# Kernel tuning notes

Measured on AMD Instinct MI355X. Metric: run time of the kernel, lower is better.

## Reference

```python
import jax, jax.numpy as jnp
import numpy as np

N_QUBITS = 8
EMBED_DIM = 1024
FFN_DIM = 4096


def setup_inputs() -> dict:
    key = jax.random.key(0)
    ks = jax.random.split(key, 6)
    x = jax.random.normal(ks[0], (8, 4096, EMBED_DIM), dtype=jnp.float32)
    # trainable RY rotation angles, one per wire (torchquantum RY has_params=True)
    theta = jax.random.normal(ks[1], (N_QUBITS,), dtype=jnp.float32)
    # torch nn.Linear params: W [out, in], b [out]
    W1 = jax.random.normal(ks[2], (FFN_DIM, N_QUBITS), dtype=jnp.float32) / np.sqrt(N_QUBITS)
    b1 = jnp.zeros((FFN_DIM,), dtype=jnp.float32)
    W2 = jax.random.normal(ks[3], (EMBED_DIM, FFN_DIM), dtype=jnp.float32) / np.sqrt(FFN_DIM)
    b2 = jnp.zeros((EMBED_DIM,), dtype=jnp.float32)
    return {"x": x, "theta": theta, "W1": W1, "b1": b1, "W2": W2, "b2": b2}


def reference(x, theta, W1, b1, W2, b2):
    # Quantum layer: per token, encoder resets state to |0..0>, applies RX(x_i)
    # on wire i, then trainable RY(theta_i), then measures <Z_i>. The circuit has
    # no entangling gates, so it factorizes per wire with the closed form:
    #   <Z_i> = cos(theta_i) * cos(x[..., i])
    # (RY(t)RX(a)|0> gives <Z> = cos t * cos a). Vectorized over batch and seq.
    q = jnp.cos(theta) * jnp.cos(x[..., :N_QUBITS])   # [B, S, n_qubits]
    # dropout is identity in eval mode
    h = jax.nn.relu(jnp.einsum('bsq,fq->bsf', q, W1) + b1)  # [B, S, ffn]
    out = jnp.einsum('bsf,ef->bse', h, W2) + b2              # [B, S, embed]
    return out
```

## Files before the change

### kernel.cpp

```cpp
#include <hip/hip_runtime.h>
#include <cstdint>
#include <cstddef>


#define M_TOT 32768L
#define N_DIM 1024
#define K_DIM 4096
#define BM 256
#define BN 256
#define BK 64
#define NT_K (K_DIM / BK)
#define CM_MAX 16384L

typedef __attribute__((ext_vector_type(8))) short short8;
typedef __attribute__((ext_vector_type(4))) float f32x4;

__device__ __forceinline__ uint16_t f2bf(float f) {
  uint32_t u = __builtin_bit_cast(uint32_t, f);
  uint32_t r = (u + 0x7fffu + ((u >> 16) & 1u)) >> 16;
  return (uint16_t)r;
}

__device__ __forceinline__ void gload_lds16(const void* gsrc, void* ldst) {
  __builtin_amdgcn_global_load_lds(
      (const __attribute__((address_space(1))) void*)gsrc,
      (__attribute__((address_space(3))) void*)ldst, 16, 0, 0);
}

__global__ __launch_bounds__(256) void prep_w2(const float* __restrict__ W2,
                                               uint16_t* __restrict__ W2sw) {
  long idx = (long)blockIdx.x * 256 + threadIdx.x;
  long e8 = idx * 8;
  int e = (int)(e8 >> 12);
  int k = (int)(e8 & 4095);
  float4 v0 = *(const float4*)(W2 + e8);
  float4 v1 = *(const float4*)(W2 + e8 + 4);
  union { uint16_t u[8]; uint4 v; } pk;
  pk.u[0] = f2bf(v0.x); pk.u[1] = f2bf(v0.y); pk.u[2] = f2bf(v0.z); pk.u[3] = f2bf(v0.w);
  pk.u[4] = f2bf(v1.x); pk.u[5] = f2bf(v1.y); pk.u[6] = f2bf(v1.z); pk.u[7] = f2bf(v1.w);
  int sg = ((k >> 3) & 7) ^ (e & 7);
  uint16_t* dst = W2sw + (long)e * 4096 + (k & ~63) + sg * 8;
  *(uint4*)dst = pk.v;
}

__global__ __launch_bounds__(256) void h_kernel(const float* __restrict__ x,
                                                const float* __restrict__ theta,
                                                const float* __restrict__ W1,
                                                const float* __restrict__ b1,
                                                uint16_t* __restrict__ Hsw) {
  __shared__ float qs[32][8];
  int tid = threadIdx.x;
  long m0 = (long)blockIdx.x * 32;
  int g = blockIdx.y * 256 + tid;
  int f0 = g * 8;

  {
    int t = tid >> 3, i = tid & 7;
    qs[t][i] = __cosf(theta[i]) * cosf(x[(m0 + t) * 1024 + i]);
  }
  __syncthreads();

  float4 w[16];
#pragma unroll
  for (int j = 0; j < 8; ++j) {
    w[2 * j]     = *(const float4*)(W1 + (long)(f0 + j) * 8);
    w[2 * j + 1] = *(const float4*)(W1 + (long)(f0 + j) * 8 + 4);
  }
  float bb[8];
#pragma unroll
  for (int j = 0; j < 8; ++j) bb[j] = b1[f0 + j];

  int blk = (g >> 3) * 64;
  int gw = g & 7;

#pragma unroll 4
  for (int t = 0; t < 32; ++t) {
    long m = m0 + t;
    float q0 = qs[t][0], q1 = qs[t][1], q2 = qs[t][2], q3 = qs[t][3];
    float q4 = qs[t][4], q5 = qs[t][5], q6 = qs[t][6], q7 = qs[t][7];
    union { uint16_t u[8]; uint4 v; } pk;
#pragma unroll
    for (int j = 0; j < 8; ++j) {
      float h = bb[j];
      h += q0 * w[2 * j].x + q1 * w[2 * j].y + q2 * w[2 * j].z + q3 * w[2 * j].w;
      h += q4 * w[2 * j + 1].x + q5 * w[2 * j + 1].y + q6 * w[2 * j + 1].z + q7 * w[2 * j + 1].w;
      h = fmaxf(h, 0.0f);
      pk.u[j] = f2bf(h);
    }
    int sg = gw ^ ((int)m & 7);
    *(uint4*)&Hsw[m * K_DIM + blk + sg * 8] = pk.v;
  }
}

__global__ __launch_bounds__(512, 2) void gemm_kernel(const uint16_t* __restrict__ Hsw,
                                                      const uint16_t* __restrict__ W2sw,
                                                      const float* __restrict__ b2,
                                                      float* __restrict__ out) {
  __shared__ uint16_t LA[2 * BM * BK];
  __shared__ uint16_t LB[2 * BN * BK];

  int nwg = gridDim.x;
  int bid = blockIdx.x;
  int sw = bid;
  if ((nwg & 7) == 0) { int cpx = nwg >> 3; sw = (bid & 7) * cpx + (bid >> 3); }
  const int NTN = N_DIM / BN;
  int mt = sw / NTN;
  int nt = sw - mt * NTN;
  long m0 = (long)mt * BM;
  int n0 = nt * BN;

  int tid = threadIdx.x;
  int lane = tid & 63;
  int wave_m = (tid >> 6) >> 2;
  int wave_n = (tid >> 6) & 3;
  int wmB = wave_m * 128;
  int wnB = wave_n * 64;

  int r  = lane & 15;
  int kq = lane >> 4;
  int xr = r & 7;

  int rowS = tid >> 3;
  int colS = (tid & 7) * 8;
  const uint16_t* srcA = Hsw  + (m0 + rowS) * K_DIM + colS;
  const uint16_t* srcB = W2sw + ((long)(n0 + rowS)) * K_DIM + colS;
  int ldsWB = (tid & ~63) * 8;

#define STAGE_A(p, h, j, t) \
  gload_lds16(srcA + (long)((h)*128 + (j)*64) * K_DIM + (t)*BK, \
              &LA[(p)*16384 + ((h)*128 + (j)*64)*BK + ldsWB])
#define STAGE_B(p, h, j, t) \
  gload_lds16(srcB + (long)((h)*128 + (j)*64) * K_DIM + (t)*BK, \
              &LB[(p)*16384 + ((h)*128 + (j)*64)*BK + ldsWB])

#define BAR() do { asm volatile("" ::: "memory"); __builtin_amdgcn_s_barrier(); \
                   asm volatile("" ::: "memory"); } while (0)
#define SGB(m_, n_) __builtin_amdgcn_sched_group_barrier((m_), (n_), 0)

#define LDA_F(p, mf_, ks_) \
  (*(const short8*)&LA[(p)*16384 + (wmB + (mf_)*16 + r)*BK + ((((ks_)*4 + kq) ^ xr)*8)])
#define LDB_F(p, nf_, ks_) \
  (*(const short8*)&LB[(p)*16384 + (wnB + (nf_)*16 + r)*BK + ((((ks_)*4 + kq) ^ xr)*8)])

#define MFMA_Q(AARR, BARR, mh, nh) do { \
    _Pragma("unroll") for (int i_ = 0; i_ < 4; ++i_) \
    _Pragma("unroll") for (int j_ = 0; j_ < 2; ++j_) \
    _Pragma("unroll") for (int ks_ = 0; ks_ < 2; ++ks_) \
      acc[(mh)*4 + i_][(nh)*2 + j_] = __builtin_amdgcn_mfma_f32_16x16x32_bf16( \
          AARR[i_][ks_], BARR[j_][ks_], acc[(mh)*4 + i_][(nh)*2 + j_], 0, 0, 0); \
  } while (0)

#define READ_B1V(p) do { \
    _Pragma("unroll") for (int j_ = 0; j_ < 2; ++j_) \
    _Pragma("unroll") for (int ks_ = 0; ks_ < 2; ++ks_) \
      b1v[j_][ks_] = LDB_F(p, 2 + j_, ks_); \
  } while (0)
#define READ_A1(p) do { \
    _Pragma("unroll") for (int i_ = 0; i_ < 4; ++i_) \
    _Pragma("unroll") for (int ks_ = 0; ks_ < 2; ++ks_) \
      a1[i_][ks_] = LDA_F(p, 4 + i_, ks_); \
  } while (0)
#define READ_A0(pn) do { \
    _Pragma("unroll") for (int i_ = 0; i_ < 4; ++i_) \
    _Pragma("unroll") for (int ks_ = 0; ks_ < 2; ++ks_) \
      a0[i_][ks_] = LDA_F(pn, i_, ks_); \
  } while (0)
#define READ_B0(pn) do { \
    _Pragma("unroll") for (int j_ = 0; j_ < 2; ++j_) \
    _Pragma("unroll") for (int ks_ = 0; ks_ < 2; ++ks_) \
      b0[j_][ks_] = LDB_F(pn, j_, ks_); \
  } while (0)

  f32x4 acc[8][4];
#pragma unroll
  for (int i = 0; i < 8; ++i)
#pragma unroll
    for (int j = 0; j < 4; ++j) acc[i][j] = (f32x4){0.f, 0.f, 0.f, 0.f};

  short8 a0[4][2];
  short8 a1[4][2];
  short8 b0[2][2];
  short8 b1v[2][2];

#pragma unroll
  for (int h = 0; h < 2; ++h)
#pragma unroll
    for (int j = 0; j < 2; ++j) STAGE_A(0, h, j, 0);
#pragma unroll
  for (int h = 0; h < 2; ++h)
#pragma unroll
    for (int j = 0; j < 2; ++j) STAGE_B(0, h, j, 0);
#pragma unroll
  for (int h = 0; h < 2; ++h)
#pragma unroll
    for (int j = 0; j < 2; ++j) STAGE_A(1, h, j, 1);
#pragma unroll
  for (int h = 0; h < 2; ++h)
#pragma unroll
    for (int j = 0; j < 2; ++j) STAGE_B(1, h, j, 1);
  asm volatile("s_waitcnt vmcnt(8)" ::: "memory");
  BAR();
  READ_A0(0);
  READ_B0(0);

#pragma unroll 2
  for (int u = 0; u < NT_K; ++u) {
    int p = u & 1;
    int tc = (u + 2 < NT_K) ? (u + 2) : (NT_K - 1);

    MFMA_Q(a0, b0, 0, 0);
    READ_B1V(p);
    READ_A1(p);
#pragma unroll
    for (int s_ = 0; s_ < 12; ++s_) { SGB(0x8, 1); SGB(0x100, 1); }
    SGB(0x8, 4);
    BAR();

    STAGE_A(p, 0, 0, tc); STAGE_A(p, 1, 0, tc);
    STAGE_B(p, 0, 0, tc); STAGE_B(p, 0, 1, tc);
    STAGE_B(p, 1, 0, tc); STAGE_B(p, 1, 1, tc);
    MFMA_Q(a0, b1v, 0, 1);
    MFMA_Q(a1, b1v, 1, 1);
#pragma unroll
    for (int s_ = 0; s_ < 6; ++s_) { SGB(0x10, 1); SGB(0x8, 5); }
    SGB(0x8, 2);
    if (u < NT_K - 2)       { asm volatile("s_waitcnt vmcnt(6)" ::: "memory"); }
    else if (u == NT_K - 2) { asm volatile("s_waitcnt vmcnt(0)" ::: "memory"); }
    BAR();

    READ_A0(p ^ 1);
    MFMA_Q(a1, b0, 1, 0);
    READ_B0(p ^ 1);
    STAGE_A(p, 0, 1, tc); STAGE_A(p, 1, 1, tc);
#pragma unroll
    for (int s_ = 0; s_ < 8; ++s_) { SGB(0x8, 1); SGB(0x100, 1); }
    SGB(0x10, 2); SGB(0x8, 8); SGB(0x100, 4);
    BAR();
  }

  float bb[4];
#pragma unroll
  for (int nf = 0; nf < 4; ++nf) bb[nf] = b2[n0 + wnB + nf * 16 + r];
  long mbase = m0 + wmB + kq * 4;
#pragma unroll
  for (int mf = 0; mf < 8; ++mf) {
#pragma unroll
    for (int nf = 0; nf < 4; ++nf) {
      int n = n0 + wnB + nf * 16 + r;
#pragma unroll
      for (int rg = 0; rg < 4; ++rg) {
        out[(mbase + mf * 16 + rg) * N_DIM + n] = acc[mf][nf][rg] + bb[nf];
      }
    }
  }
#undef STAGE_A
#undef STAGE_B
#undef BAR
#undef SGB
#undef LDA_F
#undef LDB_F
#undef MFMA_Q
#undef READ_B1V
#undef READ_A1
#undef READ_A0
#undef READ_B0
}

extern "C" void kernel_launch(void* const* d_in, const int* in_sizes, int n_in,
                              void* d_out, int out_size, void* d_ws, size_t ws_size,
                              hipStream_t stream) {
  const float* x     = (const float*)d_in[0];
  const float* theta = (const float*)d_in[1];
  const float* W1    = (const float*)d_in[2];
  const float* b1    = (const float*)d_in[3];
  const float* W2    = (const float*)d_in[4];
  const float* b2    = (const float*)d_in[5];
  float* out = (float*)d_out;

  const size_t W2SW_BYTES = (size_t)N_DIM * K_DIM * 2;
  uint16_t* W2sw = (uint16_t*)d_ws;
  uint16_t* Hsw  = (uint16_t*)((char*)d_ws + W2SW_BYTES);

  size_t avail = ws_size > W2SW_BYTES ? ws_size - W2SW_BYTES : 0;
  long CM = (long)(avail / ((size_t)K_DIM * 2));
  CM &= ~255L;
  if (CM > CM_MAX) CM = CM_MAX;
  if (CM < 256) CM = 256;

  prep_w2<<<2048, 256, 0, stream>>>(W2, W2sw);

  for (long m0 = 0; m0 < M_TOT; m0 += CM) {
    long mc = M_TOT - m0;
    if (mc > CM) mc = CM;
    dim3 gA((unsigned)(mc / 32), 2);
    h_kernel<<<gA, 256, 0, stream>>>(x + m0 * N_DIM, theta, W1, b1, Hsw);
    unsigned ngb = (unsigned)((mc / BM) * (N_DIM / BN));
    gemm_kernel<<<ngb, 512, 0, stream>>>(Hsw, W2sw, b2, out + m0 * N_DIM);
  }
}
```

Before: 298.4 us.

## Restructure GEMM main loop into barrier-phased MFMA clusters with priority boosts

```diff
diff --git a/kernel.cpp b/kernel.cpp
--- a/kernel.cpp
+++ b/kernel.cpp
@@ -135,7 +135,8 @@
 
 #define BAR() do { asm volatile("" ::: "memory"); __builtin_amdgcn_s_barrier(); \
                    asm volatile("" ::: "memory"); } while (0)
-#define SGB(m_, n_) __builtin_amdgcn_sched_group_barrier((m_), (n_), 0)
+#define LG0() do { asm volatile("s_waitcnt lgkmcnt(0)" ::: "memory"); \
+                   __builtin_amdgcn_sched_barrier(0); } while (0)
 
 #define LDA_F(p, mf_, ks_) \
   (*(const short8*)&LA[(p)*16384 + (wmB + (mf_)*16 + r)*BK + ((((ks_)*4 + kq) ^ xr)*8)])
@@ -143,11 +144,13 @@
   (*(const short8*)&LB[(p)*16384 + (wnB + (nf_)*16 + r)*BK + ((((ks_)*4 + kq) ^ xr)*8)])
 
 #define MFMA_Q(AARR, BARR, mh, nh) do { \
+    __builtin_amdgcn_s_setprio(1); \
     _Pragma("unroll") for (int i_ = 0; i_ < 4; ++i_) \
     _Pragma("unroll") for (int j_ = 0; j_ < 2; ++j_) \
     _Pragma("unroll") for (int ks_ = 0; ks_ < 2; ++ks_) \
       acc[(mh)*4 + i_][(nh)*2 + j_] = __builtin_amdgcn_mfma_f32_16x16x32_bf16( \
           AARR[i_][ks_], BARR[j_][ks_], acc[(mh)*4 + i_][(nh)*2 + j_], 0, 0, 0); \
+    __builtin_amdgcn_s_setprio(0); \
   } while (0)
 
 #define READ_B1V(p) do { \
@@ -200,43 +203,44 @@
     for (int j = 0; j < 2; ++j) STAGE_B(1, h, j, 1);
   asm volatile("s_waitcnt vmcnt(8)" ::: "memory");
   BAR();
-  READ_A0(0);
-  READ_B0(0);
 
 #pragma unroll 2
   for (int u = 0; u < NT_K; ++u) {
     int p = u & 1;
     int tc = (u + 2 < NT_K) ? (u + 2) : (NT_K - 1);
 
+    READ_A0(p);
+    READ_B0(p);
+    asm volatile("s_waitcnt lgkmcnt(8)" ::: "memory");
+    BAR();
+    LG0();
     MFMA_Q(a0, b0, 0, 0);
+    BAR();
+
     READ_B1V(p);
+    STAGE_A(p, 0, 0, tc); STAGE_A(p, 1, 0, tc);
+    BAR();
+    LG0();
+    MFMA_Q(a0, b1v, 0, 1);
+    BAR();
+
     READ_A1(p);
-#pragma unroll
-    for (int s_ = 0; s_ < 12; ++s_) { SGB(0x8, 1); SGB(0x100, 1); }
-    SGB(0x8, 4);
-    BAR();
-
-    STAGE_A(p, 0, 0, tc); STAGE_A(p, 1, 0, tc);
     STAGE_B(p, 0, 0, tc); STAGE_B(p, 0, 1, tc);
     STAGE_B(p, 1, 0, tc); STAGE_B(p, 1, 1, tc);
-    MFMA_Q(a0, b1v, 0, 1);
+    BAR();
+    LG0();
     MFMA_Q(a1, b1v, 1, 1);
-#pragma unroll
-    for (int s_ = 0; s_ < 6; ++s_) { SGB(0x10, 1); SGB(0x8, 5); }
-    SGB(0x8, 2);
     if (u < NT_K - 2)       { asm volatile("s_waitcnt vmcnt(6)" ::: "memory"); }
     else if (u == NT_K - 2) { asm volatile("s_waitcnt vmcnt(0)" ::: "memory"); }
     BAR();
 
-    READ_A0(p ^ 1);
+    STAGE_A(p, 0, 1, tc); STAGE_A(p, 1, 1, tc);
+    BAR();
+    LG0();
     MFMA_Q(a1, b0, 1, 0);
-    READ_B0(p ^ 1);
-    STAGE_A(p, 0, 1, tc); STAGE_A(p, 1, 1, tc);
-#pragma unroll
-    for (int s_ = 0; s_ < 8; ++s_) { SGB(0x8, 1); SGB(0x100, 1); }
-    SGB(0x10, 2); SGB(0x8, 8); SGB(0x100, 4);
-    BAR();
-  }
+    BAR();
+  }
+  asm volatile("s_waitcnt vmcnt(0)" ::: "memory");
 
   float bb[4];
 #pragma unroll
@@ -256,7 +260,7 @@
 #undef STAGE_A
 #undef STAGE_B
 #undef BAR
-#undef SGB
+#undef LG0
 #undef LDA_F
 #undef LDB_F
 #undef MFMA_Q
```

New measurement: 340.0 us. 1.14x slower.
